# Kernel tuning notes

Hardware: AMD Instinct MI355X
Metric: run time of the kernel (lower is better)

## Reference

```python
import jax, jax.numpy as jnp
import numpy as np

HID = 2880
NQ = 64
NKV = 8
HD = 64
THETA = 150000.0
WINDOW = 128
S = 8192


def _rope(x, positions):
    # x: [S, H, D]; half-split (rotate_half) convention
    d = x.shape[-1]
    inv_freq = 1.0 / (THETA ** (jnp.arange(0, d, 2, dtype=jnp.float32) / d))  # [D/2]
    ang = positions.astype(jnp.float32)[:, None] * inv_freq[None, :]          # [S, D/2]
    cos = jnp.cos(ang)[:, None, :]
    sin = jnp.sin(ang)[:, None, :]
    x1, x2 = jnp.split(x, 2, axis=-1)
    return jnp.concatenate([x1 * cos - x2 * sin, x2 * cos + x1 * sin], axis=-1)


def setup_inputs() -> dict:
    key = jax.random.key(0)
    ks = jax.random.split(key, 12)
    sd = 0.02
    return {
        "hidden": jax.random.normal(ks[0], (S, HID), dtype=jnp.float32),
        "positions": jnp.arange(S, dtype=jnp.int64) if jax.config.jax_enable_x64 else jnp.arange(S, dtype=jnp.int32),
        "Wq": jax.random.normal(ks[1], (HID, NQ * HD), dtype=jnp.float32) * sd,
        "bq": jax.random.normal(ks[2], (NQ * HD,), dtype=jnp.float32) * sd,
        "Wk": jax.random.normal(ks[3], (HID, NKV * HD), dtype=jnp.float32) * sd,
        "bk": jax.random.normal(ks[4], (NKV * HD,), dtype=jnp.float32) * sd,
        "Wv": jax.random.normal(ks[5], (HID, NKV * HD), dtype=jnp.float32) * sd,
        "bv": jax.random.normal(ks[6], (NKV * HD,), dtype=jnp.float32) * sd,
        "Wo": jax.random.normal(ks[7], (NQ * HD, HID), dtype=jnp.float32) * sd,
        "bo": jax.random.normal(ks[8], (HID,), dtype=jnp.float32) * sd,
    }


def _attention(hidden, positions, Wq, bq, Wk, bk, Wv, bv, Wo, bo):
    n_tok = hidden.shape[0]
    q = (hidden @ Wq + bq).reshape(n_tok, NQ, HD)
    k = (hidden @ Wk + bk).reshape(n_tok, NKV, HD)
    v = (hidden @ Wv + bv).reshape(n_tok, NKV, HD)
    q = _rope(q, positions)
    k = _rope(k, positions)

    # Blocked sliding-window causal attention (window == block size W).
    W = WINDOW
    nb = n_tok // W
    group = NQ // NKV
    qb = q.reshape(nb, W, NQ, HD)
    kb = k.reshape(nb, W, NKV, HD)
    vb = v.reshape(nb, W, NKV, HD)
    # each query block attends to its own block plus the previous one (2W keys)
    k_prev = jnp.concatenate([jnp.zeros_like(kb[:1]), kb[:-1]], axis=0)
    v_prev = jnp.concatenate([jnp.zeros_like(vb[:1]), vb[:-1]], axis=0)
    k_ctx = jnp.concatenate([k_prev, kb], axis=1)   # [nb, 2W, NKV, HD]
    v_ctx = jnp.concatenate([v_prev, vb], axis=1)
    # GQA: repeat KV heads to match query heads
    k_ctx = jnp.repeat(k_ctx, group, axis=2)        # [nb, 2W, NQ, HD]
    v_ctx = jnp.repeat(v_ctx, group, axis=2)

    scale = 1.0 / np.sqrt(HD)
    scores = jnp.einsum('bqhd,bkhd->bhqk', qb, k_ctx) * scale  # [nb, NQ, W, 2W]

    qi = jnp.arange(W)[:, None]            # local query pos
    ki = jnp.arange(2 * W)[None, :]        # local key pos within context
    diff = qi - ki + W                     # i - j (global)
    band = (diff >= 0) & (diff < WINDOW)   # causal + window
    kpos = jnp.arange(nb)[:, None, None] * W + ki[None] - W  # global key pos
    mask = band[None] & (kpos >= 0)        # [nb, W, 2W]

    neg = jnp.finfo(scores.dtype).min
    scores = jnp.where(mask[:, None, :, :], scores, neg)
    p = jax.nn.softmax(scores, axis=-1)
    attn = jnp.einsum('bhqk,bkhd->bqhd', p, v_ctx)  # [nb, W, NQ, HD]
    attn = attn.reshape(n_tok, NQ * HD)
    return attn @ Wo + bo


def reference(hidden, positions, Wq, bq, Wk, bk, Wv, bv, Wo, bo):
    return _attention(hidden, positions, Wq, bq, Wk, bk, Wv, bv, Wo, bo)
```

## Files before the change

kernel.cpp:

```cpp
#include <hip/hip_runtime.h>
#include <stdint.h>

#define S_TOK 8192
#define HID 2880
#define NQ 64
#define NKV 8
#define HD 64
#define QKV_N 5120
#define NO_PAD 2944

typedef __attribute__((ext_vector_type(8))) __bf16 bf16x8;
typedef __attribute__((ext_vector_type(8))) short short8;
typedef __attribute__((ext_vector_type(4))) float f32x4;

__device__ __forceinline__ unsigned short f2bf(float f) {
  unsigned int u = __builtin_bit_cast(unsigned int, f);
  u += 0x7fff + ((u >> 16) & 1);
  return (unsigned short)(u >> 16);
}
__device__ __forceinline__ float bf2f(unsigned short h) {
  unsigned int u = ((unsigned int)h) << 16;
  return __builtin_bit_cast(float, u);
}

__device__ __forceinline__ void async_lds16(const void* g, void* l) {
  __builtin_amdgcn_global_load_lds(
      (const __attribute__((address_space(1))) unsigned int*)g,
      (__attribute__((address_space(3))) unsigned int*)l, 16, 0, 0);
}

__global__ __launch_bounds__(256) void cvt_bf16_kernel(
    const float* __restrict__ src, unsigned short* __restrict__ dst) {
  size_t i = ((size_t)blockIdx.x * 256 + threadIdx.x) * 8;
  float4 a = *(const float4*)(src + i);
  float4 b = *(const float4*)(src + i + 4);
  union { unsigned short u[8]; uint4 v; } o;
  o.u[0] = f2bf(a.x); o.u[1] = f2bf(a.y); o.u[2] = f2bf(a.z); o.u[3] = f2bf(a.w);
  o.u[4] = f2bf(b.x); o.u[5] = f2bf(b.y); o.u[6] = f2bf(b.z); o.u[7] = f2bf(b.w);
  *(uint4*)(dst + i) = o.v;
}

__global__ __launch_bounds__(256) void transpose_cvt(
    const float* __restrict__ src, unsigned short* __restrict__ dst,
    int R, int C, int rowOff) {
  __shared__ float tile[32][33];
  int tx = threadIdx.x, ty = threadIdx.y;
  int c0 = blockIdx.x * 32, r0 = blockIdx.y * 32;
#pragma unroll
  for (int i = 0; i < 4; ++i)
    tile[ty + i * 8][tx] = src[(size_t)(r0 + ty + i * 8) * C + c0 + tx];
  __syncthreads();
#pragma unroll
  for (int i = 0; i < 4; ++i)
    dst[(size_t)(c0 + ty + i * 8 + rowOff) * R + r0 + tx] = f2bf(tile[tx][ty + i * 8]);
}

__global__ __launch_bounds__(256) void rope_kernel(
    unsigned short* __restrict__ qkv, const int* __restrict__ positions) {
  int gid = blockIdx.x * 256 + threadIdx.x;
  int d = gid & 31;
  int rest = gid >> 5;
  int head = rest % 72;
  int t = rest / 72;
  unsigned short* p = qkv + (size_t)t * QKV_N + head * 64;
  float x1 = bf2f(p[d]);
  float x2 = bf2f(p[d + 32]);
  float pos = (float)positions[t];
  float inv = exp2f(-0.5373313430f * (float)d);
  float ang = pos * inv;
  float s, c;
  __sincosf(ang, &s, &c);
  s = sinf(ang); c = cosf(ang);
  p[d] = f2bf(x1 * c - x2 * s);
  p[d + 32] = f2bf(x2 * c + x1 * s);
}

template <int MODE>
__global__ __launch_bounds__(256) void gemm_bt(
    const unsigned short* __restrict__ A, const unsigned short* __restrict__ BT,
    void* __restrict__ Cout, int K,
    const float* __restrict__ b0, const float* __restrict__ b1,
    const float* __restrict__ b2) {
  __shared__ unsigned short As[128 * 64];
  __shared__ unsigned short Bs[128 * 64];
  const int tid = threadIdx.x;
  const int wave = tid >> 6, lane = tid & 63;
  const int quad = lane >> 4, ml = lane & 15;
  const int wy = wave >> 1, wx = wave & 1;
  const int m0 = blockIdx.y * 128, n0 = blockIdx.x * 128;

  f32x4 zero = {0.f, 0.f, 0.f, 0.f};
  f32x4 acc[4][4];
#pragma unroll
  for (int i = 0; i < 4; ++i)
#pragma unroll
    for (int j = 0; j < 4; ++j) acc[i][j] = zero;

  const int srow = tid >> 3;
  const int scol = (tid & 7) << 3;

  for (int k0 = 0; k0 < K; k0 += 64) {
    const unsigned short* Ag = A + (size_t)m0 * K + k0;
    const unsigned short* Bg = BT + (size_t)n0 * K + k0;
#pragma unroll
    for (int i = 0; i < 4; ++i) {
      int s = tid + i * 256;
      int row = s >> 3, c = (s & 7) << 3;
      async_lds16(Ag + (size_t)row * K + c, &As[s * 8]);
      async_lds16(Bg + (size_t)row * K + c, &Bs[s * 8]);
    }
    __syncthreads();
#pragma unroll
    for (int kk = 0; kk < 2; ++kk) {
      bf16x8 af[4];
#pragma unroll
      for (int i = 0; i < 4; ++i)
        af[i] = *(const bf16x8*)&As[(wy * 64 + i * 16 + ml) * 64 + kk * 32 + quad * 8];
#pragma unroll
      for (int j = 0; j < 4; ++j) {
        bf16x8 bfr = *(const bf16x8*)&Bs[(wx * 64 + j * 16 + ml) * 64 + kk * 32 + quad * 8];
#pragma unroll
        for (int i = 0; i < 4; ++i)
          acc[i][j] = __builtin_amdgcn_mfma_f32_16x16x32_bf16(af[i], bfr, acc[i][j], 0, 0, 0);
      }
    }
    __syncthreads();
  }

#pragma unroll
  for (int j = 0; j < 4; ++j) {
    int col = n0 + wx * 64 + j * 16 + ml;
    float bias;
    if (MODE == 0) {
      bias = (col < 4096) ? b0[col] : (col < 4608 ? b1[col - 4096] : b2[col - 4608]);
    } else {
      bias = (col < HID) ? b0[col] : 0.f;
    }
#pragma unroll
    for (int i = 0; i < 4; ++i) {
#pragma unroll
      for (int r = 0; r < 4; ++r) {
        int row = m0 + wy * 64 + i * 16 + quad * 4 + r;
        float v = acc[i][j][r] + bias;
        if (MODE == 0) {
          ((unsigned short*)Cout)[(size_t)row * QKV_N + col] = f2bf(v);
        } else {
          if (col < HID) ((float*)Cout)[(size_t)row * HID + col] = v;
        }
      }
    }
  }
}

__global__ __launch_bounds__(256) void attn_kernel(
    const unsigned short* __restrict__ qkv, unsigned short* __restrict__ attn) {
  __shared__ unsigned short Qs[64 * 72];
  __shared__ unsigned short Ks[192 * 72];
  __shared__ unsigned short VTs[64 * 200];

  const int tid = threadIdx.x;
  const int B = blockIdx.x;
  const int h = blockIdx.y;
  const int hk = h >> 3;
  const int wave = tid >> 6, lane = tid & 63;
  const int quad = lane >> 4, ml = lane & 15;

#pragma unroll
  for (int it = 0; it < 2; ++it) {
    int s = tid + it * 256;
    int row = s >> 3, c = (s & 7) << 3;
    *(uint4*)&Qs[row * 72 + c] =
        *(const uint4*)(qkv + (size_t)(B * 64 + row) * QKV_N + h * 64 + c);
  }
#pragma unroll
  for (int it = 0; it < 6; ++it) {
    int s = tid + it * 256;
    int j = s >> 3, c = (s & 7) << 3;
    int tk = B * 64 - 128 + j;
    uint4 kv = make_uint4(0, 0, 0, 0), vv = make_uint4(0, 0, 0, 0);
    if (tk >= 0) {
      kv = *(const uint4*)(qkv + (size_t)tk * QKV_N + 4096 + hk * 64 + c);
      vv = *(const uint4*)(qkv + (size_t)tk * QKV_N + 4608 + hk * 64 + c);
    }
    *(uint4*)&Ks[j * 72 + c] = kv;
    union { uint4 q; unsigned short u[8]; } vu;
    vu.q = vv;
#pragma unroll
    for (int e = 0; e < 8; ++e) VTs[(c + e) * 200 + j] = vu.u[e];
  }
  __syncthreads();

  f32x4 zero = {0.f, 0.f, 0.f, 0.f};
  f32x4 sc[12];
#pragma unroll
  for (int jn = 0; jn < 12; ++jn) sc[jn] = zero;
#pragma unroll
  for (int kk = 0; kk < 2; ++kk) {
    bf16x8 af = *(const bf16x8*)&Qs[(wave * 16 + ml) * 72 + kk * 32 + quad * 8];
#pragma unroll
    for (int jn = 0; jn < 12; ++jn) {
      bf16x8 bfr = *(const bf16x8*)&Ks[(jn * 16 + ml) * 72 + kk * 32 + quad * 8];
      sc[jn] = __builtin_amdgcn_mfma_f32_16x16x32_bf16(af, bfr, sc[jn], 0, 0, 0);
    }
  }

  const float NEG = -3.0e38f;
  float mx[4], sm[4];
#pragma unroll
  for (int r = 0; r < 4; ++r) mx[r] = NEG;
#pragma unroll
  for (int jn = 0; jn < 12; ++jn) {
    int j = jn * 16 + ml;
#pragma unroll
    for (int r = 0; r < 4; ++r) {
      int i = wave * 16 + quad * 4 + r;
      bool valid = (j > i) && (j <= i + 128) && (B * 64 + j - 128 >= 0);
      float v = valid ? sc[jn][r] * 0.125f : NEG;
      sc[jn][r] = v;
      mx[r] = fmaxf(mx[r], v);
    }
  }
#pragma unroll
  for (int r = 0; r < 4; ++r) {
#pragma unroll
    for (int off = 1; off < 16; off <<= 1)
      mx[r] = fmaxf(mx[r], __shfl_xor(mx[r], off, 64));
    sm[r] = 0.f;
  }
#pragma unroll
  for (int jn = 0; jn < 12; ++jn) {
#pragma unroll
    for (int r = 0; r < 4; ++r) {
      float p = expf(sc[jn][r] - mx[r]);
      sc[jn][r] = p;
      sm[r] += p;
    }
  }
#pragma unroll
  for (int r = 0; r < 4; ++r) {
#pragma unroll
    for (int off = 1; off < 16; off <<= 1) sm[r] += __shfl_xor(sm[r], off, 64);
    sm[r] = 1.0f / sm[r];
  }
  __syncthreads();

  unsigned short* P = Ks;
#pragma unroll
  for (int jn = 0; jn < 12; ++jn) {
#pragma unroll
    for (int r = 0; r < 4; ++r)
      P[(wave * 16 + quad * 4 + r) * 200 + jn * 16 + ml] = f2bf(sc[jn][r] * sm[r]);
  }
  __syncthreads();

  f32x4 ov[4];
#pragma unroll
  for (int jn = 0; jn < 4; ++jn) ov[jn] = zero;
#pragma unroll
  for (int ks = 0; ks < 6; ++ks) {
    bf16x8 af = *(const bf16x8*)&P[(wave * 16 + ml) * 200 + ks * 32 + quad * 8];
#pragma unroll
    for (int jn = 0; jn < 4; ++jn) {
      bf16x8 bfr = *(const bf16x8*)&VTs[(jn * 16 + ml) * 200 + ks * 32 + quad * 8];
      ov[jn] = __builtin_amdgcn_mfma_f32_16x16x32_bf16(af, bfr, ov[jn], 0, 0, 0);
    }
  }
#pragma unroll
  for (int jn = 0; jn < 4; ++jn) {
#pragma unroll
    for (int r = 0; r < 4; ++r) {
      int row = B * 64 + wave * 16 + quad * 4 + r;
      attn[(size_t)row * 4096 + h * 64 + jn * 16 + ml] = f2bf(ov[jn][r]);
    }
  }
}

extern "C" void kernel_launch(void* const* d_in, const int* in_sizes, int n_in,
                              void* d_out, int out_size, void* d_ws, size_t ws_size,
                              hipStream_t stream) {
  const float* hidden = (const float*)d_in[0];
  const int* positions = (const int*)d_in[1];
  const float* Wq = (const float*)d_in[2];
  const float* bq = (const float*)d_in[3];
  const float* Wk = (const float*)d_in[4];
  const float* bk = (const float*)d_in[5];
  const float* Wv = (const float*)d_in[6];
  const float* bv = (const float*)d_in[7];
  const float* Wo = (const float*)d_in[8];
  const float* bo = (const float*)d_in[9];
  float* out = (float*)d_out;

  char* ws = (char*)d_ws;
  unsigned short* A_h   = (unsigned short*)(ws);
  unsigned short* BTqkv = (unsigned short*)(ws + 47185920);
  unsigned short* qkv   = (unsigned short*)(ws + 76677120);
  unsigned short* BTo   = (unsigned short*)(ws + 160563200);
  unsigned short* attn  = (unsigned short*)(ws);

  cvt_bf16_kernel<<<11520, 256, 0, stream>>>(hidden, A_h);
  dim3 tb(32, 8);
  transpose_cvt<<<dim3(128, 90), tb, 0, stream>>>(Wq, BTqkv, HID, 4096, 0);
  transpose_cvt<<<dim3(16, 90), tb, 0, stream>>>(Wk, BTqkv, HID, 512, 4096);
  transpose_cvt<<<dim3(16, 90), tb, 0, stream>>>(Wv, BTqkv, HID, 512, 4608);
  transpose_cvt<<<dim3(90, 128), tb, 0, stream>>>(Wo, BTo, 4096, HID, 0);
  hipMemsetAsync(BTo + (size_t)HID * 4096, 0, (size_t)(NO_PAD - HID) * 4096 * 2, stream);

  gemm_bt<0><<<dim3(QKV_N / 128, S_TOK / 128), 256, 0, stream>>>(
      A_h, BTqkv, qkv, HID, bq, bk, bv);
  rope_kernel<<<73728, 256, 0, stream>>>(qkv, positions);
  attn_kernel<<<dim3(S_TOK / 64, NQ), 256, 0, stream>>>(qkv, attn);
  gemm_bt<1><<<dim3(NO_PAD / 128, S_TOK / 128), 256, 0, stream>>>(
      attn, BTo, out, 4096, bo, nullptr, nullptr);
}
```

Baseline: 1.085 ms.

## Use 32x32x16 MFMA with XOR-swizzled LDS and staged coalesced bf16 epilogue

The GEMM inner loop moves from 16x16x32 MFMA tiles to 32x32x16 tiles with a 2x2 accumulator per wave. This halves the fragment loads per MFMA. LDS tiles are now XOR-swizzled on the 16-byte chunk index to avoid bank conflicts on fragment reads. The QKV GEMM epilogue stages results through LDS and writes them with 16-byte coalesced stores instead of scattered 2-byte stores, at the cost of an extra barrier and an LDS round trip. The rope kernel also drops a redundant __sincosf call.

Result: faster. 969.7 us (-10.7%).

```diff
diff --git a/kernel.cpp b/kernel.cpp
--- a/kernel.cpp
+++ b/kernel.cpp
@@ -10,8 +10,8 @@
 #define NO_PAD 2944
 
 typedef __attribute__((ext_vector_type(8))) __bf16 bf16x8;
-typedef __attribute__((ext_vector_type(8))) short short8;
 typedef __attribute__((ext_vector_type(4))) float f32x4;
+typedef __attribute__((ext_vector_type(16))) float f32x16;
 
 __device__ __forceinline__ unsigned short f2bf(float f) {
   unsigned int u = __builtin_bit_cast(unsigned int, f);
@@ -68,9 +68,7 @@
   float pos = (float)positions[t];
   float inv = exp2f(-0.5373313430f * (float)d);
   float ang = pos * inv;
-  float s, c;
-  __sincosf(ang, &s, &c);
-  s = sinf(ang); c = cosf(ang);
+  float s = sinf(ang), c = cosf(ang);
   p[d] = f2bf(x1 * c - x2 * s);
   p[d + 32] = f2bf(x2 * c + x1 * s);
 }
@@ -81,23 +79,22 @@
     void* __restrict__ Cout, int K,
     const float* __restrict__ b0, const float* __restrict__ b1,
     const float* __restrict__ b2) {
-  __shared__ unsigned short As[128 * 64];
-  __shared__ unsigned short Bs[128 * 64];
+  __shared__ unsigned short lds[128 * 128];
+  unsigned short* As = lds;
+  unsigned short* Bs = lds + 128 * 64;
   const int tid = threadIdx.x;
   const int wave = tid >> 6, lane = tid & 63;
-  const int quad = lane >> 4, ml = lane & 15;
+  const int l31 = lane & 31, lh = lane >> 5;
   const int wy = wave >> 1, wx = wave & 1;
   const int m0 = blockIdx.y * 128, n0 = blockIdx.x * 128;
 
-  f32x4 zero = {0.f, 0.f, 0.f, 0.f};
-  f32x4 acc[4][4];
-#pragma unroll
-  for (int i = 0; i < 4; ++i)
-#pragma unroll
-    for (int j = 0; j < 4; ++j) acc[i][j] = zero;
-
-  const int srow = tid >> 3;
-  const int scol = (tid & 7) << 3;
+  f32x16 acc[2][2];
+#pragma unroll
+  for (int i = 0; i < 2; ++i)
+#pragma unroll
+    for (int j = 0; j < 2; ++j)
+#pragma unroll
+      for (int r = 0; r < 16; ++r) acc[i][j][r] = 0.f;
 
   for (int k0 = 0; k0 < K; k0 += 64) {
     const unsigned short* Ag = A + (size_t)m0 * K + k0;
@@ -105,47 +102,75 @@
 #pragma unroll
     for (int i = 0; i < 4; ++i) {
       int s = tid + i * 256;
-      int row = s >> 3, c = (s & 7) << 3;
-      async_lds16(Ag + (size_t)row * K + c, &As[s * 8]);
-      async_lds16(Bg + (size_t)row * K + c, &Bs[s * 8]);
+      int row = s >> 3;
+      int c = (s & 7) ^ (row & 7);
+      async_lds16(Ag + (size_t)row * K + c * 8, &As[s * 8]);
+      async_lds16(Bg + (size_t)row * K + c * 8, &Bs[s * 8]);
     }
     __syncthreads();
 #pragma unroll
-    for (int kk = 0; kk < 2; ++kk) {
-      bf16x8 af[4];
-#pragma unroll
-      for (int i = 0; i < 4; ++i)
-        af[i] = *(const bf16x8*)&As[(wy * 64 + i * 16 + ml) * 64 + kk * 32 + quad * 8];
-#pragma unroll
-      for (int j = 0; j < 4; ++j) {
-        bf16x8 bfr = *(const bf16x8*)&Bs[(wx * 64 + j * 16 + ml) * 64 + kk * 32 + quad * 8];
-#pragma unroll
-        for (int i = 0; i < 4; ++i)
-          acc[i][j] = __builtin_amdgcn_mfma_f32_16x16x32_bf16(af[i], bfr, acc[i][j], 0, 0, 0);
+    for (int ks = 0; ks < 4; ++ks) {
+      bf16x8 af[2], bfr[2];
+#pragma unroll
+      for (int ra = 0; ra < 2; ++ra) {
+        int row = wy * 64 + ra * 32 + l31;
+        int p = (ks * 2 + lh) ^ (row & 7);
+        af[ra] = *(const bf16x8*)&As[row * 64 + p * 8];
       }
+#pragma unroll
+      for (int cb = 0; cb < 2; ++cb) {
+        int row = wx * 64 + cb * 32 + l31;
+        int p = (ks * 2 + lh) ^ (row & 7);
+        bfr[cb] = *(const bf16x8*)&Bs[row * 64 + p * 8];
+      }
+#pragma unroll
+      for (int ra = 0; ra < 2; ++ra)
+#pragma unroll
+        for (int cb = 0; cb < 2; ++cb)
+          acc[ra][cb] = __builtin_amdgcn_mfma_f32_32x32x16_bf16(
+              af[ra], bfr[cb], acc[ra][cb], 0, 0, 0);
     }
     __syncthreads();
   }
 
-#pragma unroll
-  for (int j = 0; j < 4; ++j) {
-    int col = n0 + wx * 64 + j * 16 + ml;
-    float bias;
-    if (MODE == 0) {
-      bias = (col < 4096) ? b0[col] : (col < 4608 ? b1[col - 4096] : b2[col - 4608]);
-    } else {
-      bias = (col < HID) ? b0[col] : 0.f;
-    }
-#pragma unroll
-    for (int i = 0; i < 4; ++i) {
-#pragma unroll
-      for (int r = 0; r < 4; ++r) {
-        int row = m0 + wy * 64 + i * 16 + quad * 4 + r;
-        float v = acc[i][j][r] + bias;
-        if (MODE == 0) {
-          ((unsigned short*)Cout)[(size_t)row * QKV_N + col] = f2bf(v);
-        } else {
-          if (col < HID) ((float*)Cout)[(size_t)row * HID + col] = v;
+  if (MODE == 0) {
+#pragma unroll
+    for (int cb = 0; cb < 2; ++cb) {
+      int col = wx * 64 + cb * 32 + l31;
+      int gcol = n0 + col;
+      float bias = (gcol < 4096) ? b0[gcol]
+                                 : (gcol < 4608 ? b1[gcol - 4096] : b2[gcol - 4608]);
+#pragma unroll
+      for (int ra = 0; ra < 2; ++ra) {
+#pragma unroll
+        for (int r = 0; r < 16; ++r) {
+          int row = wy * 64 + ra * 32 + (r & 3) + 8 * (r >> 2) + 4 * lh;
+          lds[row * 128 + col] = f2bf(acc[ra][cb][r] + bias);
+        }
+      }
+    }
+    __syncthreads();
+    unsigned short* C16 = (unsigned short*)Cout;
+#pragma unroll
+    for (int i = 0; i < 8; ++i) {
+      int s = tid + i * 256;
+      int row = s >> 4, cc = (s & 15) * 8;
+      *(uint4*)(C16 + (size_t)(m0 + row) * QKV_N + n0 + cc) =
+          *(const uint4*)&lds[row * 128 + cc];
+    }
+  } else {
+#pragma unroll
+    for (int cb = 0; cb < 2; ++cb) {
+      int gcol = n0 + wx * 64 + cb * 32 + l31;
+      if (gcol < HID) {
+        float bias = b0[gcol];
+#pragma unroll
+        for (int ra = 0; ra < 2; ++ra) {
+#pragma unroll
+          for (int r = 0; r < 16; ++r) {
+            int row = m0 + wy * 64 + ra * 32 + (r & 3) + 8 * (r >> 2) + 4 * lh;
+            ((float*)Cout)[(size_t)row * HID + gcol] = acc[ra][cb][r] + bias;
+          }
         }
       }
     }
```
